# Kernel optimization log

Measured on AMD Instinct MI355X. Metric: run time of the kernel, lower is better.

Reference implementation:

```python
import jax, jax.numpy as jnp
import numpy as np

T_TYPES = 4      # node types
N_NODES = 8192   # nodes per type
D_IN = 256       # init_dim
H = 256          # hidden_dim
D_OUT = 64       # out_dim
N_LAYERS = 2     # args.trans_num
TEMP = 1.0       # args.search_temp


def _conv1d(x, w, b):
    # x: [T, N, Din] -> Conv1d over node axis (torch: data[j].T -> Conv1d -> .T)
    # w: [Dout, Din, 3], b: [Dout]
    y = jax.lax.conv_general_dilated(
        jnp.swapaxes(x, 1, 2), w, window_strides=(1,), padding=((1, 1),),
        dimension_numbers=('NCH', 'OIH', 'NCH'))
    return jnp.swapaxes(y + b[None, :, None], 1, 2)  # [T, N, Dout]


def _rel_conv1d(x, w, b):
    # per-type conv kernels: w [T, Dout, Din, 3], b [T, Dout]
    return jax.vmap(lambda xi, wi, bi: _conv1d(xi[None], wi, bi)[0])(x, w, b)


def setup_inputs() -> dict:
    key = jax.random.key(0)
    ks = jax.random.split(key, 16)
    s = 1.0 / np.sqrt(H)  # keep relu chains numerically tame
    return {
        'x': jax.random.normal(ks[0], (T_TYPES, N_NODES, D_IN), jnp.float32),
        'lin1_w': jax.random.normal(ks[1], (D_IN, H), jnp.float32) * s,
        'lin1_b': jax.random.normal(ks[2], (H,), jnp.float32) * 0.01,
        'lin_w': jax.random.normal(ks[3], (N_LAYERS, H, H), jnp.float32) * s,
        'lin_b': jax.random.normal(ks[4], (N_LAYERS, H), jnp.float32) * 0.01,
        'rel_lin_w': jax.random.normal(ks[5], (N_LAYERS, T_TYPES, H, H), jnp.float32) * s,
        'rel_lin_b': jax.random.normal(ks[6], (N_LAYERS, T_TYPES, H), jnp.float32) * 0.01,
        'conv_w': jax.random.normal(ks[7], (N_LAYERS, H, H, 3), jnp.float32) * s,
        'conv_b': jax.random.normal(ks[8], (N_LAYERS, H), jnp.float32) * 0.01,
        'rel_conv_w': jax.random.normal(ks[9], (N_LAYERS, T_TYPES, H, H, 3), jnp.float32) * s,
        'rel_conv_b': jax.random.normal(ks[10], (N_LAYERS, T_TYPES, H), jnp.float32) * 0.01,
        'out_w': jax.random.normal(ks[11], (H, D_OUT), jnp.float32) * s,
        'out_b': jax.random.normal(ks[12], (D_OUT,), jnp.float32) * 0.01,
        'trans_arch': jax.random.normal(ks[13], (N_LAYERS, 5), jnp.float32),
        'agg_arch': jax.random.normal(ks[14], (3,), jnp.float32),
    }


def reference(x, lin1_w, lin1_b, lin_w, lin_b, rel_lin_w, rel_lin_b,
              conv_w, conv_b, rel_conv_w, rel_conv_b, out_w, out_b,
              trans_arch, agg_arch):
    relu = jax.nn.relu
    tw = jax.nn.softmax(trans_arch / TEMP, axis=-1)  # [L, 5]
    aw = jax.nn.softmax(agg_arch / TEMP)             # [3]

    # input projection (lin1)
    h = jnp.einsum('tnd,de->tne', x, lin1_w) + lin1_b  # [T, N, H]

    for l in range(N_LAYERS):
        # TRANS_OPTION = ['linear','rel-linear','conv','rel-conv','identity']
        o_lin = relu(jnp.einsum('tnd,de->tne', h, lin_w[l]) + lin_b[l])
        o_rlin = relu(jnp.einsum('tnd,tde->tne', h, rel_lin_w[l]) + rel_lin_b[l][:, None, :])
        o_conv = relu(_conv1d(h, conv_w[l], conv_b[l]))
        o_rconv = relu(_rel_conv1d(h, rel_conv_w[l], rel_conv_b[l]))
        w = tw[l]
        h = w[0] * o_lin + w[1] * o_rlin + w[2] * o_conv + w[3] * o_rconv + w[4] * h

    # Agg_Op: concat all types along node axis, AGG_OPTION = ['sum','mean','max']
    flat = h.reshape(-1, H)  # [T*N, H]
    agg = aw[0] * flat.sum(axis=0) + aw[1] * flat.mean(axis=0) + aw[2] * flat.max(axis=0)

    # reconstructed output head (class body truncated in source)
    return agg @ out_w + out_b  # [D_OUT]
```

## Files before the change

kernel.cpp:

```cpp
#include <hip/hip_runtime.h>
#include <hip/hip_bf16.h>
#include <math.h>

#define NN 8192
#define HP 8194
#define HD 256
#define DOUT 64

typedef __bf16 bf16_t;
typedef __bf16 bf16x8 __attribute__((ext_vector_type(8)));
typedef float f32x4 __attribute__((ext_vector_type(4)));

#define H0_OFF 0ull
#define H1_OFF 16781312ull
#define PW_OFF 33562624ull
#define TW_OFF 38936576ull
#define PS_OFF 38936832ull
#define PM_OFF 39198976ull
#define PS2_OFF H1_OFF
#define PM2_OFF (H1_OFF + 65536ull)
#define PWG_L1 0
#define PWG_SH(l) (8192 + (l)*32768)
#define PWG_TY(l) (73728 + (l)*131072)

__device__ __forceinline__ void glds16(const void* g, void* l) {
    __builtin_amdgcn_global_load_lds(
        (const __attribute__((address_space(1))) void*)g,
        (__attribute__((address_space(3))) void*)l, 16, 0, 0);
}

__device__ __forceinline__ float frelu(float v) { return v > 0.f ? v : 0.f; }

__global__ __launch_bounds__(256) void pack_kernel(
    const float* __restrict__ lin1_w, const float* __restrict__ lin_w,
    const float* __restrict__ rel_lin_w, const float* __restrict__ conv_w,
    const float* __restrict__ rel_conv_w, const float* __restrict__ trans_arch,
    const float* __restrict__ agg_arch, bf16_t* __restrict__ pw,
    float* __restrict__ tws, bf16_t* __restrict__ h0, bf16_t* __restrict__ h1) {
    __shared__ float lt[32 * 257];
    const int tid = threadIdx.x, bx = blockIdx.x;
    if (bx < 88) {
        int m = bx >> 3, kt = bx & 7;
        const float* src; size_t img; bool l1 = (m == 0);
        if (m == 0) { src = lin1_w; img = 0; }
        else if (m <= 2) { int l = m - 1; src = lin_w + (size_t)l * 65536; img = PWG_SH(l); }
        else { int u = m - 3; int l = u >> 2, tt = u & 3;
            src = rel_lin_w + (size_t)(l * 4 + tt) * 65536;
            img = PWG_TY(l) + (size_t)tt * 32768; }
        const float4* s4 = (const float4*)(src + (size_t)kt * 32 * 256);
#pragma unroll
        for (int i = 0; i < 8; ++i) {
            int idx = tid + 256 * i;
            float4 v = s4[idx];
            int k = idx >> 6, n = (idx * 4) & 255;
            float* p = &lt[k * 257 + n];
            p[0] = v.x; p[1] = v.y; p[2] = v.z; p[3] = v.w;
        }
        __syncthreads();
        int j2 = tid >> 6, lq = (tid >> 4) & 3, lrow = tid & 15;
#pragma unroll
        for (int ct = 0; ct < 4; ++ct) {
            int n = ct * 64 + j2 * 16 + lrow;
            bf16x8 wv;
#pragma unroll
            for (int e = 0; e < 8; ++e) wv[e] = (bf16_t)lt[(lq * 8 + e) * 257 + n];
            size_t g = l1 ? (img + (size_t)kt * 1024 + ct * 256 + tid)
                          : (img + (size_t)kt * 4096 + ct * 1024 + tid);
            *(bf16x8*)(pw + g * 8) = wv;
        }
    } else if (bx < 408) {
        int idx = bx - 88;
        int inst = idx >> 5, r = idx & 31, kt = r >> 2, ct = r & 3;
        const float* src; size_t img;
        if (inst < 2) { src = conv_w + (size_t)inst * 196608; img = PWG_SH(inst); }
        else { int u = inst - 2; int l = u >> 2, tt = u & 3;
            src = rel_conv_w + (size_t)(l * 4 + tt) * 196608;
            img = PWG_TY(l) + (size_t)tt * 32768; }
        {
            int rl = tid >> 2, q0 = tid & 3;
            int n = ct * 64 + rl;
            const float4* rb = (const float4*)(src) + (size_t)n * 192 + kt * 24;
#pragma unroll
            for (int i = 0; i < 6; ++i) {
                float4 v = rb[q0 + 4 * i];
                float* p = &lt[rl * 100 + (q0 + 4 * i) * 4];
                p[0] = v.x; p[1] = v.y; p[2] = v.z; p[3] = v.w;
            }
        }
        __syncthreads();
        int j2 = tid >> 6, lq = (tid >> 4) & 3, lrow = tid & 15;
        int nl = j2 * 16 + lrow;
#pragma unroll
        for (int s = 1; s <= 3; ++s) {
            bf16x8 wv;
#pragma unroll
            for (int e = 0; e < 8; ++e) wv[e] = (bf16_t)lt[nl * 100 + (lq * 8 + e) * 3 + (s - 1)];
            size_t g = img + (size_t)kt * 4096 + ct * 1024 + s * 256 + tid;
            *(bf16x8*)(pw + g * 8) = wv;
        }
    } else if (bx == 408) {
        for (int i = tid; i < 4096; i += 256) {
            int row_id = i >> 8, col = i & 255;
            int buf = row_id >> 3, t_ = (row_id >> 1) & 3, side = row_id & 1;
            bf16_t* hb = buf ? h1 : h0;
            hb[((size_t)t_ * HP + (side ? (HP - 1) : 0)) * HD + col] = (bf16_t)0.f;
        }
    } else {
        if (tid == 0) {
            for (int l = 0; l < 2; ++l) {
                float m = trans_arch[l * 5];
                for (int i = 1; i < 5; ++i) m = fmaxf(m, trans_arch[l * 5 + i]);
                float e[5], s = 0.f;
                for (int i = 0; i < 5; ++i) { e[i] = __expf(trans_arch[l * 5 + i] - m); s += e[i]; }
                for (int i = 0; i < 5; ++i) tws[l * 5 + i] = e[i] / s;
            }
            float m = fmaxf(fmaxf(agg_arch[0], agg_arch[1]), agg_arch[2]);
            float e0 = __expf(agg_arch[0] - m), e1 = __expf(agg_arch[1] - m), e2 = __expf(agg_arch[2] - m);
            float s = e0 + e1 + e2;
            tws[10] = e0 / s; tws[11] = e1 / s; tws[12] = e2 / s;
        }
    }
}

__device__ __forceinline__ void load_af(bf16x8 af[4], const bf16_t* lA,
                                        int sh, int wm, int lrow, int lq) {
#pragma unroll
    for (int i = 0; i < 4; ++i)
        af[i] = *(const bf16x8*)&lA[(sh + wm + i * 16 + lrow) * 40 + lq * 8];
}

__device__ __forceinline__ void do_mat(const bf16x8 af[4], const bf16_t* Bb,
                                       int grpbase, int lane, f32x4 acc[4][2]) {
#pragma unroll
    for (int j = 0; j < 2; ++j) {
        bf16x8 bfr = *(const bf16x8*)&Bb[(grpbase + j) * 512 + lane * 8];
#pragma unroll
        for (int i = 0; i < 4; ++i)
            acc[i][j] = __builtin_amdgcn_mfma_f32_16x16x32_bf16(af[i], bfr, acc[i][j], 0, 0, 0);
    }
}

__global__ __launch_bounds__(256, 2) void lin1_kernel(
    const float* __restrict__ x, bf16_t* __restrict__ h0,
    const bf16_t* __restrict__ pwL1, const float* __restrict__ b) {
    __shared__ __align__(16) bf16_t lA[64 * 40];
    __shared__ __align__(16) bf16_t lB[8192];
    const int tid = threadIdx.x, lane = tid & 63, wid = tid >> 6;
    const int bx = blockIdx.x;
    const int t = bx >> 7, mt = bx & 127;
    const int m0 = mt * 64;
    const int lrow = lane & 15, lq = lane >> 4;
    const int r0 = tid >> 2, kq0 = tid & 3;
    const float* xT = x + (size_t)t * NN * HD + (size_t)(m0 + r0) * HD + kq0 * 8;

    f32x4 acc[4][4];
#pragma unroll
    for (int i = 0; i < 4; ++i)
#pragma unroll
        for (int j = 0; j < 4; ++j) acc[i][j] = (f32x4){0.f, 0.f, 0.f, 0.f};

    float4 px0, px1;
    { const float4* p = (const float4*)xT; px0 = p[0]; px1 = p[1]; }

    for (int kt = 0; kt < 8; ++kt) {
        __syncthreads();
        bf16x8 wv;
        wv[0]=(bf16_t)px0.x; wv[1]=(bf16_t)px0.y; wv[2]=(bf16_t)px0.z; wv[3]=(bf16_t)px0.w;
        wv[4]=(bf16_t)px1.x; wv[5]=(bf16_t)px1.y; wv[6]=(bf16_t)px1.z; wv[7]=(bf16_t)px1.w;
        *(bf16x8*)&lA[r0 * 40 + kq0 * 8] = wv;
#pragma unroll
        for (int j2 = 0; j2 < 4; ++j2) {
            const bf16_t* src = pwL1 + ((size_t)kt * 1024 + wid * 256 + j2 * 64) * 8 + (size_t)lane * 8;
            glds16(src, &lB[(wid * 4 + j2) * 512]);
        }
        if (kt < 7) {
            const float4* p = (const float4*)(xT + (kt + 1) * 32);
            px0 = p[0]; px1 = p[1];
        }
        __syncthreads();
        bf16x8 af[4];
#pragma unroll
        for (int i = 0; i < 4; ++i)
            af[i] = *(const bf16x8*)&lA[(i * 16 + lrow) * 40 + lq * 8];
#pragma unroll
        for (int j = 0; j < 4; ++j) {
            bf16x8 bfr = *(const bf16x8*)&lB[(wid * 4 + j) * 512 + lane * 8];
#pragma unroll
            for (int i = 0; i < 4; ++i)
                acc[i][j] = __builtin_amdgcn_mfma_f32_16x16x32_bf16(af[i], bfr, acc[i][j], 0, 0, 0);
        }
    }
    size_t obase = (size_t)t * HP * HD + (size_t)(1 + m0) * HD;
#pragma unroll
    for (int j = 0; j < 4; ++j) {
        int col = wid * 64 + j * 16 + lrow;
        float bj = b[col];
#pragma unroll
        for (int i = 0; i < 4; ++i)
#pragma unroll
            for (int r = 0; r < 4; ++r) {
                int orow = i * 16 + lq * 4 + r;
                h0[obase + (size_t)orow * HD + col] = (bf16_t)(acc[i][j][r] + bj);
            }
    }
}

template <int DO_RED>
__global__ __launch_bounds__(256, 2) void layer_kernel(
    const bf16_t* __restrict__ hin, bf16_t* __restrict__ hout,
    const bf16_t* __restrict__ pwS, const bf16_t* __restrict__ pwT,
    const float* __restrict__ lin_b, const float* __restrict__ rel_lin_b,
    const float* __restrict__ conv_b, const float* __restrict__ rel_conv_b,
    const float* __restrict__ tw5, float* __restrict__ ps, float* __restrict__ pm) {
    __shared__ __align__(16) bf16_t lA[130 * 40];
    __shared__ __align__(16) bf16_t lB[16384];
    __shared__ float lsum[4][64], lmax[4][64];
    const int tid = threadIdx.x, lane = tid & 63, wid = tid >> 6;
    const int bx = blockIdx.x;
    const int xcd = bx & 7, q = bx >> 3;
    const int ct = q & 3, tm = (q >> 2) * 8 + xcd;
    const int t = tm >> 6, mt = tm & 63;
    const int m0 = mt * 128, c0 = ct * 64;
    const int wm = (wid >> 1) * 64, wn = (wid & 1) * 32;
    const int lrow = lane & 15, lq = lane >> 4;
    const int wj2 = wn >> 4;
    const bf16_t* aG = hin + (size_t)t * HP * HD + (size_t)m0 * HD;
    const bf16_t* pwTt = pwT + (size_t)t * 262144;
    const int r0 = tid >> 1, kq0 = (tid & 1) * 2;
    const int r1 = 128 + (tid >> 1);
    const bool tail = (tid < 4);

    f32x4 acc[4][4][2];
#pragma unroll
    for (int m = 0; m < 4; ++m)
#pragma unroll
        for (int i = 0; i < 4; ++i)
#pragma unroll
            for (int j = 0; j < 2; ++j) acc[m][i][j] = (f32x4){0.f, 0.f, 0.f, 0.f};

    bf16x8 pa0, pa1, pb0, pb1;
    pa0 = *(const bf16x8*)(aG + (size_t)r0 * HD + kq0 * 8);
    pa1 = *(const bf16x8*)(aG + (size_t)r0 * HD + kq0 * 8 + 8);
    if (tail) {
        pb0 = *(const bf16x8*)(aG + (size_t)r1 * HD + kq0 * 8);
        pb1 = *(const bf16x8*)(aG + (size_t)r1 * HD + kq0 * 8 + 8);
    }
    for (int kt = 0; kt < 8; ++kt) {
        __syncthreads();
        *(bf16x8*)&lA[r0 * 40 + kq0 * 8] = pa0;
        *(bf16x8*)&lA[r0 * 40 + kq0 * 8 + 8] = pa1;
        if (tail) {
            *(bf16x8*)&lA[r1 * 40 + kq0 * 8] = pb0;
            *(bf16x8*)&lA[r1 * 40 + kq0 * 8 + 8] = pb1;
        }
#pragma unroll
        for (int qq = 0; qq < 8; ++qq) {
            int tk = wid * 8 + qq, half = tk >> 4, grp = tk & 15;
            const bf16_t* src = (half ? pwTt : pwS) + (size_t)((kt * 4 + ct) * 16 + grp) * 512 + (size_t)lane * 8;
            glds16(src, &lB[(half * 16 + grp) * 512]);
        }
        if (kt < 7) {
            pa0 = *(const bf16x8*)(aG + (size_t)r0 * HD + (kt + 1) * 32 + kq0 * 8);
            pa1 = *(const bf16x8*)(aG + (size_t)r0 * HD + (kt + 1) * 32 + kq0 * 8 + 8);
            if (tail) {
                pb0 = *(const bf16x8*)(aG + (size_t)r1 * HD + (kt + 1) * 32 + kq0 * 8);
                pb1 = *(const bf16x8*)(aG + (size_t)r1 * HD + (kt + 1) * 32 + kq0 * 8 + 8);
            }
        }
        __syncthreads();
        bf16x8 af[4];
        load_af(af, lA, 1, wm, lrow, lq);
        do_mat(af, lB, 0 + 0 + wj2, lane, acc[0]);
        do_mat(af, lB, 16 + 0 + wj2, lane, acc[1]);
        do_mat(af, lB, 0 + 8 + wj2, lane, acc[2]);
        do_mat(af, lB, 16 + 8 + wj2, lane, acc[3]);
        load_af(af, lA, 0, wm, lrow, lq);
        do_mat(af, lB, 0 + 4 + wj2, lane, acc[2]);
        do_mat(af, lB, 16 + 4 + wj2, lane, acc[3]);
        load_af(af, lA, 2, wm, lrow, lq);
        do_mat(af, lB, 0 + 12 + wj2, lane, acc[2]);
        do_mat(af, lB, 16 + 12 + wj2, lane, acc[3]);
    }
    const float w0 = tw5[0], w1 = tw5[1], w2 = tw5[2], w3 = tw5[3], w4 = tw5[4];
    const float* rb1 = rel_lin_b + t * 256;
    const float* rb3 = rel_conv_b + t * 256;
    size_t obase = (size_t)t * HP * HD + (size_t)(1 + m0) * HD;
    float csum[2], cmax[2];
#pragma unroll
    for (int j = 0; j < 2; ++j) { csum[j] = 0.f; cmax[j] = -3.4e38f; }
#pragma unroll
    for (int j = 0; j < 2; ++j) {
        int col = c0 + wn + j * 16 + lrow;
        float b0 = lin_b[col], b1 = rb1[col], b2 = conv_b[col], b3 = rb3[col];
#pragma unroll
        for (int i = 0; i < 4; ++i)
#pragma unroll
            for (int r = 0; r < 4; ++r) {
                int orow = wm + i * 16 + lq * 4 + r;
                size_t idx = obase + (size_t)orow * HD + col;
                float v = w0 * frelu(acc[0][i][j][r] + b0)
                        + w1 * frelu(acc[1][i][j][r] + b1)
                        + w2 * frelu(acc[2][i][j][r] + b2)
                        + w3 * frelu(acc[3][i][j][r] + b3)
                        + w4 * (float)hin[idx];
                hout[idx] = (bf16_t)v;
                if (DO_RED) { csum[j] += v; cmax[j] = fmaxf(cmax[j], v); }
            }
    }
    if (DO_RED) {
#pragma unroll
        for (int j = 0; j < 2; ++j) {
            csum[j] += __shfl_xor(csum[j], 16, 64);
            csum[j] += __shfl_xor(csum[j], 32, 64);
            float o1 = __shfl_xor(cmax[j], 16, 64); cmax[j] = fmaxf(cmax[j], o1);
            float o2 = __shfl_xor(cmax[j], 32, 64); cmax[j] = fmaxf(cmax[j], o2);
        }
        __syncthreads();
        if (lq == 0) {
#pragma unroll
            for (int j = 0; j < 2; ++j) {
                lsum[wid][wn + j * 16 + lrow] = csum[j];
                lmax[wid][wn + j * 16 + lrow] = cmax[j];
            }
        }
        __syncthreads();
        if (tid < 64) {
            int w0i = tid >> 5;
            float S = lsum[w0i][tid] + lsum[w0i + 2][tid];
            float M = fmaxf(lmax[w0i][tid], lmax[w0i + 2][tid]);
            int g = t * 64 + mt;
            ps[g * 256 + c0 + tid] = S;
            pm[g * 256 + c0 + tid] = M;
        }
    }
}

__global__ __launch_bounds__(256) void reduce2a_kernel(
    const float* __restrict__ ps, const float* __restrict__ pm,
    float* __restrict__ ps2, float* __restrict__ pm2) {
    int c = threadIdx.x, b = blockIdx.x;
    float s = 0.f, m = -3.4e38f;
#pragma unroll
    for (int i = 0; i < 4; ++i) {
        int g = b * 4 + i;
        s += ps[g * 256 + c];
        m = fmaxf(m, pm[g * 256 + c]);
    }
    ps2[b * 256 + c] = s;
    pm2[b * 256 + c] = m;
}

__global__ __launch_bounds__(256) void reduce2b_kernel(
    const float* __restrict__ ps2, const float* __restrict__ pm2,
    const float* __restrict__ out_w, const float* __restrict__ out_b,
    const float* __restrict__ tws, float* __restrict__ out) {
    __shared__ float aggL[256];
    int c = threadIdx.x;
    float s = 0.f, m = -3.4e38f;
#pragma unroll 4
    for (int g = 0; g < 64; ++g) {
        s += ps2[g * 256 + c];
        m = fmaxf(m, pm2[g * 256 + c]);
    }
    float aw0 = tws[10], aw1 = tws[11], aw2 = tws[12];
    aggL[c] = aw0 * s + aw1 * (s * (1.0f / 32768.f)) + aw2 * m;
    __syncthreads();
    if (c < DOUT) {
        float o = out_b[c];
        for (int e = 0; e < 256; ++e) o += aggL[e] * out_w[e * DOUT + c];
        out[c] = o;
    }
}

extern "C" void kernel_launch(void* const* d_in, const int* in_sizes, int n_in,
                              void* d_out, int out_size, void* d_ws, size_t ws_size,
                              hipStream_t stream) {
    const float* x          = (const float*)d_in[0];
    const float* lin1_w     = (const float*)d_in[1];
    const float* lin1_b     = (const float*)d_in[2];
    const float* lin_w      = (const float*)d_in[3];
    const float* lin_b      = (const float*)d_in[4];
    const float* rel_lin_w  = (const float*)d_in[5];
    const float* rel_lin_b  = (const float*)d_in[6];
    const float* conv_w     = (const float*)d_in[7];
    const float* conv_b     = (const float*)d_in[8];
    const float* rel_conv_w = (const float*)d_in[9];
    const float* rel_conv_b = (const float*)d_in[10];
    const float* out_w      = (const float*)d_in[11];
    const float* out_b      = (const float*)d_in[12];
    const float* trans_arch = (const float*)d_in[13];
    const float* agg_arch   = (const float*)d_in[14];

    char* ws = (char*)d_ws;
    bf16_t* h0 = (bf16_t*)(ws + H0_OFF);
    bf16_t* h1 = (bf16_t*)(ws + H1_OFF);
    bf16_t* pw = (bf16_t*)(ws + PW_OFF);
    float* tws = (float*)(ws + TW_OFF);
    float* ps  = (float*)(ws + PS_OFF);
    float* pm  = (float*)(ws + PM_OFF);
    float* ps2 = (float*)(ws + PS2_OFF);
    float* pm2 = (float*)(ws + PM2_OFF);
    float* outp = (float*)d_out;

    pack_kernel<<<410, 256, 0, stream>>>(lin1_w, lin_w, rel_lin_w, conv_w, rel_conv_w,
                                         trans_arch, agg_arch, pw, tws, h0, h1);
    lin1_kernel<<<512, 256, 0, stream>>>(x, h0, pw + (size_t)PWG_L1 * 8, lin1_b);
    layer_kernel<0><<<1024, 256, 0, stream>>>(h0, h1,
        pw + (size_t)PWG_SH(0) * 8, pw + (size_t)PWG_TY(0) * 8,
        lin_b, rel_lin_b, conv_b, rel_conv_b, tws, nullptr, nullptr);
    layer_kernel<1><<<1024, 256, 0, stream>>>(h1, h0,
        pw + (size_t)PWG_SH(1) * 8, pw + (size_t)PWG_TY(1) * 8,
        lin_b + 256, rel_lin_b + 1024, conv_b + 256, rel_conv_b + 1024, tws + 5, ps, pm);
    reduce2a_kernel<<<64, 256, 0, stream>>>(ps, pm, ps2, pm2);
    reduce2b_kernel<<<1, 256, 0, stream>>>(ps2, pm2, out_w, out_b, tws, outp);
}
```

Measured before the change: 198.4 us.

## Split layer GEMM into two weight passes to cut registers and raise occupancy

The layer kernel now processes the shared weights (linear+conv) and the per-type weights (rel-linear+rel-conv) in two sequential passes, each with half the accumulators, folding each pass's ReLU/weighted result into a running sum. This roughly halves accumulator register use and LDS for B, allowing launch bounds of 3 blocks per CU. The A tile is now loaded with direct global-to-LDS copies in a k-major layout instead of register staging. In exchange, the A tile is reloaded twice per k-step across passes, there are twice as many barriers, and the register prefetch overlap is lost.

```diff
diff --git a/kernel.cpp b/kernel.cpp
--- a/kernel.cpp
+++ b/kernel.cpp
@@ -122,13 +122,6 @@
     }
 }
 
-__device__ __forceinline__ void load_af(bf16x8 af[4], const bf16_t* lA,
-                                        int sh, int wm, int lrow, int lq) {
-#pragma unroll
-    for (int i = 0; i < 4; ++i)
-        af[i] = *(const bf16x8*)&lA[(sh + wm + i * 16 + lrow) * 40 + lq * 8];
-}
-
 __device__ __forceinline__ void do_mat(const bf16x8 af[4], const bf16_t* Bb,
                                        int grpbase, int lane, f32x4 acc[4][2]) {
 #pragma unroll
@@ -206,14 +199,14 @@
 }
 
 template <int DO_RED>
-__global__ __launch_bounds__(256, 2) void layer_kernel(
+__global__ __launch_bounds__(256, 3) void layer_kernel(
     const bf16_t* __restrict__ hin, bf16_t* __restrict__ hout,
     const bf16_t* __restrict__ pwS, const bf16_t* __restrict__ pwT,
     const float* __restrict__ lin_b, const float* __restrict__ rel_lin_b,
     const float* __restrict__ conv_b, const float* __restrict__ rel_conv_b,
     const float* __restrict__ tw5, float* __restrict__ ps, float* __restrict__ pm) {
-    __shared__ __align__(16) bf16_t lA[130 * 40];
-    __shared__ __align__(16) bf16_t lB[16384];
+    __shared__ __align__(16) bf16_t lA[4 * 1040];
+    __shared__ __align__(16) bf16_t lB[8192];
     __shared__ float lsum[4][64], lmax[4][64];
     const int tid = threadIdx.x, lane = tid & 63, wid = tid >> 6;
     const int bx = blockIdx.x;
@@ -226,64 +219,73 @@
     const int wj2 = wn >> 4;
     const bf16_t* aG = hin + (size_t)t * HP * HD + (size_t)m0 * HD;
     const bf16_t* pwTt = pwT + (size_t)t * 262144;
-    const int r0 = tid >> 1, kq0 = (tid & 1) * 2;
-    const int r1 = 128 + (tid >> 1);
-    const bool tail = (tid < 4);
-
-    f32x4 acc[4][4][2];
-#pragma unroll
-    for (int m = 0; m < 4; ++m)
-#pragma unroll
-        for (int i = 0; i < 4; ++i)
-#pragma unroll
-            for (int j = 0; j < 2; ++j) acc[m][i][j] = (f32x4){0.f, 0.f, 0.f, 0.f};
-
-    bf16x8 pa0, pa1, pb0, pb1;
-    pa0 = *(const bf16x8*)(aG + (size_t)r0 * HD + kq0 * 8);
-    pa1 = *(const bf16x8*)(aG + (size_t)r0 * HD + kq0 * 8 + 8);
-    if (tail) {
-        pb0 = *(const bf16x8*)(aG + (size_t)r1 * HD + kq0 * 8);
-        pb1 = *(const bf16x8*)(aG + (size_t)r1 * HD + kq0 * 8 + 8);
-    }
-    for (int kt = 0; kt < 8; ++kt) {
-        __syncthreads();
-        *(bf16x8*)&lA[r0 * 40 + kq0 * 8] = pa0;
-        *(bf16x8*)&lA[r0 * 40 + kq0 * 8 + 8] = pa1;
-        if (tail) {
-            *(bf16x8*)&lA[r1 * 40 + kq0 * 8] = pb0;
-            *(bf16x8*)&lA[r1 * 40 + kq0 * 8 + 8] = pb1;
-        }
-#pragma unroll
-        for (int qq = 0; qq < 8; ++qq) {
-            int tk = wid * 8 + qq, half = tk >> 4, grp = tk & 15;
-            const bf16_t* src = (half ? pwTt : pwS) + (size_t)((kt * 4 + ct) * 16 + grp) * 512 + (size_t)lane * 8;
-            glds16(src, &lB[(half * 16 + grp) * 512]);
-        }
-        if (kt < 7) {
-            pa0 = *(const bf16x8*)(aG + (size_t)r0 * HD + (kt + 1) * 32 + kq0 * 8);
-            pa1 = *(const bf16x8*)(aG + (size_t)r0 * HD + (kt + 1) * 32 + kq0 * 8 + 8);
-            if (tail) {
-                pb0 = *(const bf16x8*)(aG + (size_t)r1 * HD + (kt + 1) * 32 + kq0 * 8);
-                pb1 = *(const bf16x8*)(aG + (size_t)r1 * HD + (kt + 1) * 32 + kq0 * 8 + 8);
-            }
-        }
-        __syncthreads();
-        bf16x8 af[4];
-        load_af(af, lA, 1, wm, lrow, lq);
-        do_mat(af, lB, 0 + 0 + wj2, lane, acc[0]);
-        do_mat(af, lB, 16 + 0 + wj2, lane, acc[1]);
-        do_mat(af, lB, 0 + 8 + wj2, lane, acc[2]);
-        do_mat(af, lB, 16 + 8 + wj2, lane, acc[3]);
-        load_af(af, lA, 0, wm, lrow, lq);
-        do_mat(af, lB, 0 + 4 + wj2, lane, acc[2]);
-        do_mat(af, lB, 16 + 4 + wj2, lane, acc[3]);
-        load_af(af, lA, 2, wm, lrow, lq);
-        do_mat(af, lB, 0 + 12 + wj2, lane, acc[2]);
-        do_mat(af, lB, 16 + 12 + wj2, lane, acc[3]);
-    }
-    const float w0 = tw5[0], w1 = tw5[1], w2 = tw5[2], w3 = tw5[3], w4 = tw5[4];
-    const float* rb1 = rel_lin_b + t * 256;
-    const float* rb3 = rel_conv_b + t * 256;
+
+    f32x4 res[4][2];
+#pragma unroll
+    for (int i = 0; i < 4; ++i)
+#pragma unroll
+        for (int j = 0; j < 2; ++j) res[i][j] = (f32x4){0.f, 0.f, 0.f, 0.f};
+
+    for (int p = 0; p < 2; ++p) {
+        const bf16_t* W = p ? pwTt : pwS;
+        f32x4 acc[2][4][2];
+#pragma unroll
+        for (int m = 0; m < 2; ++m)
+#pragma unroll
+            for (int i = 0; i < 4; ++i)
+#pragma unroll
+                for (int j = 0; j < 2; ++j) acc[m][i][j] = (f32x4){0.f, 0.f, 0.f, 0.f};
+
+        for (int kt = 0; kt < 8; ++kt) {
+            __syncthreads();
+            {
+                const bf16_t* asrc = aG + kt * 32 + wid * 8 + (size_t)lane * HD;
+                bf16_t* adst = &lA[wid * 1040];
+                glds16(asrc, adst);
+                glds16(asrc + (size_t)64 * HD, adst + 64 * 8);
+                glds16(asrc + (size_t)66 * HD, adst + 66 * 8);
+            }
+            {
+                const bf16_t* bbase = W + ((size_t)(kt * 4 + ct) * 16) * 512 + (size_t)lane * 8;
+#pragma unroll
+                for (int qq = 0; qq < 4; ++qq) {
+                    int grp = wid * 4 + qq;
+                    glds16(bbase + (size_t)grp * 512, &lB[grp * 512]);
+                }
+            }
+            __syncthreads();
+            bf16x8 af[4];
+#pragma unroll
+            for (int i = 0; i < 4; ++i)
+                af[i] = *(const bf16x8*)&lA[lq * 1040 + (1 + wm + i * 16 + lrow) * 8];
+            do_mat(af, lB, 0 + wj2, lane, acc[0]);
+            do_mat(af, lB, 8 + wj2, lane, acc[1]);
+#pragma unroll
+            for (int i = 0; i < 4; ++i)
+                af[i] = *(const bf16x8*)&lA[lq * 1040 + (0 + wm + i * 16 + lrow) * 8];
+            do_mat(af, lB, 4 + wj2, lane, acc[1]);
+#pragma unroll
+            for (int i = 0; i < 4; ++i)
+                af[i] = *(const bf16x8*)&lA[lq * 1040 + (2 + wm + i * 16 + lrow) * 8];
+            do_mat(af, lB, 12 + wj2, lane, acc[1]);
+        }
+        const float wA = tw5[p];
+        const float wB = tw5[2 + p];
+        const float* bA = p ? rel_lin_b + t * 256 : lin_b;
+        const float* bB = p ? rel_conv_b + t * 256 : conv_b;
+#pragma unroll
+        for (int j = 0; j < 2; ++j) {
+            int col = c0 + wn + j * 16 + lrow;
+            float ba = bA[col], bb = bB[col];
+#pragma unroll
+            for (int i = 0; i < 4; ++i)
+#pragma unroll
+                for (int r = 0; r < 4; ++r)
+                    res[i][j][r] += wA * frelu(acc[0][i][j][r] + ba)
+                                  + wB * frelu(acc[1][i][j][r] + bb);
+        }
+    }
+    const float w4 = tw5[4];
     size_t obase = (size_t)t * HP * HD + (size_t)(1 + m0) * HD;
     float csum[2], cmax[2];
 #pragma unroll
@@ -291,18 +293,13 @@
 #pragma unroll
     for (int j = 0; j < 2; ++j) {
         int col = c0 + wn + j * 16 + lrow;
-        float b0 = lin_b[col], b1 = rb1[col], b2 = conv_b[col], b3 = rb3[col];
 #pragma unroll
         for (int i = 0; i < 4; ++i)
 #pragma unroll
             for (int r = 0; r < 4; ++r) {
                 int orow = wm + i * 16 + lq * 4 + r;
                 size_t idx = obase + (size_t)orow * HD + col;
-                float v = w0 * frelu(acc[0][i][j][r] + b0)
-                        + w1 * frelu(acc[1][i][j][r] + b1)
-                        + w2 * frelu(acc[2][i][j][r] + b2)
-                        + w3 * frelu(acc[3][i][j][r] + b3)
-                        + w4 * (float)hin[idx];
+                float v = res[i][j][r] + w4 * (float)hin[idx];
                 hout[idx] = (bf16_t)v;
                 if (DO_RED) { csum[j] += v; cmax[j] = fmaxf(cmax[j], v); }
             }
```

After: 228.9 us. +15.4%, slower.
